# Performance work log

Hardware: AMD Instinct MI355X
Metric: run time of the kernel (lower is better)

The kernel has to match this reference:

```python
import jax, jax.numpy as jnp
import numpy as np

TOP_K = 2
CAPACITY_FACTOR = 1.25
AUX_LOSS_ALPHA = 0.01
Z_LOSS_ALPHA = 0.001


def setup_inputs() -> dict:
    key = jax.random.key(0)
    k1, k2, k3, k4 = jax.random.split(key, 4)
    B, S, H, I, E = 4, 2048, 1024, 4096, 8
    x = jax.random.normal(k1, (B, S, H), dtype=jnp.float32)
    # router: xavier_uniform with gain 0.1
    router_w = jax.random.normal(k2, (H, E), dtype=jnp.float32) * 0.1 * (2.0 / (H + E)) ** 0.5
    # expert weights: kaiming-ish scale 1/sqrt(fan_in)
    w1 = jax.random.normal(k3, (E, H, I), dtype=jnp.float32) * (1.0 / H) ** 0.5
    w2 = jax.random.normal(k4, (E, I, H), dtype=jnp.float32) * (1.0 / I) ** 0.5
    return {"x": x, "router_w": router_w, "w1": w1, "w2": w2}


def reference(x, router_w, w1, w2):
    B, S, H = x.shape
    E = router_w.shape[1]
    # router logits [B, S, E]
    logits = jnp.einsum('bsh,he->bse', x, router_w)
    # expert-choice: each expert picks `capacity` tokens along the seq axis
    capacity = int(min(S, max(1, (S * TOP_K) // E * CAPACITY_FACTOR)))
    topk_vals, topk_idx = jax.lax.top_k(jnp.swapaxes(logits, 1, 2), capacity)  # [B, E, C]
    topk_w = jax.nn.softmax(topk_vals, axis=-1)  # [B, E, C]
    # flat indices into [B*S] token space
    flat_idx = (jnp.arange(B)[:, None, None] * S + topk_idx).reshape(-1)  # [B*E*C]
    x_flat = x.reshape(-1, H)
    selected = x_flat[flat_idx].reshape(B, E, capacity, H)
    # per-expert SiLU MLP as grouped GEMMs
    mid = jax.nn.silu(jnp.einsum('bech,ehi->beci', selected, w1))
    expert_out = jnp.einsum('beci,eih->bech', mid, w2)
    weighted = (expert_out * topk_w[..., None]).reshape(-1, H)
    # scatter-add combine + count-based averaging
    out = jnp.zeros_like(x_flat).at[flat_idx].add(weighted)
    counts = jnp.zeros((B * S,), dtype=x.dtype).at[flat_idx].add(jnp.ones_like(flat_idx, dtype=x.dtype))
    out = (out / jnp.clip(counts, 1.0)[:, None]).reshape(B, S, H)
    # routing loss: load-balance aux + z-loss
    probs = jax.nn.softmax(logits, axis=-1)
    usage = probs.mean(axis=(0, 1))  # [E]
    aux_loss = jnp.mean((usage - 1.0 / E) ** 2) * E
    z_loss = jnp.mean(logits ** 2)
    routing_loss = AUX_LOSS_ALPHA * aux_loss + Z_LOSS_ALPHA * z_loss
    return out, routing_loss
```

## Files before the change

kernel.cpp:

```cpp
#include <hip/hip_runtime.h>
#include <hip/hip_bf16.h>
#include <stdint.h>

#define B_ 4
#define S_ 2048
#define H_ 1024
#define I_ 4096
#define E_ 8
#define CAP 640
#define NTOK (B_*S_)
#define NBE  (B_*E_)

typedef _Float16 f16;
typedef f16 f16x8 __attribute__((ext_vector_type(8)));
typedef float f32x4 __attribute__((ext_vector_type(4)));

#define OFF_LOGITS 0u
#define OFF_TOPKI  (256u*1024u)
#define OFF_TOPKW  (OFF_TOPKI + 128u*1024u)
#define OFF_COUNTS (OFF_TOPKW + 128u*1024u)
#define OFF_SCAL   (OFF_COUNTS + 64u*1024u)
#define OFF_XH     (1u<<20)
#define OFF_WT     (18u<<20)
#define OFF_MID    (86u<<20)

__device__ __forceinline__ void gl_lds16(const void* g, void* l) {
    __builtin_amdgcn_global_load_lds(
        (const __attribute__((address_space(1))) uint32_t*)g,
        (__attribute__((address_space(3))) uint32_t*)l, 16, 0, 0);
}

__global__ void k_router(const float* __restrict__ x, const float* __restrict__ rw,
                         float* __restrict__ logits, float* __restrict__ scal,
                         f16* __restrict__ xh) {
    __shared__ float rwt[E_ * H_];
    __shared__ float part[4][9];
    int tid = threadIdx.x;
    for (int i = tid; i < E_ * H_; i += 256) {
        int h = i >> 3, e = i & 7;
        rwt[e * H_ + h] = rw[i];
    }
    __syncthreads();
    int w = tid >> 6, lane = tid & 63;
    int t = blockIdx.x * 4 + w;
    const float* xr = x + (size_t)t * H_;
    f16* xhr = xh + ((size_t)t << 10);
    float acc[E_];
#pragma unroll
    for (int e = 0; e < E_; ++e) acc[e] = 0.f;
    for (int it = 0; it < H_ / 64; ++it) {
        int h = lane + it * 64;
        float xv = xr[h];
        xhr[h] = (f16)xv;
#pragma unroll
        for (int e = 0; e < E_; ++e) acc[e] += xv * rwt[e * H_ + h];
    }
#pragma unroll
    for (int off = 32; off > 0; off >>= 1)
#pragma unroll
        for (int e = 0; e < E_; ++e) acc[e] += __shfl_down(acc[e], off);
    if (lane == 0) {
        int b = t >> 11, s = t & 2047;
        float m = acc[0];
#pragma unroll
        for (int e = 1; e < E_; ++e) m = fmaxf(m, acc[e]);
        float z = 0.f, ps = 0.f;
        float p[E_];
#pragma unroll
        for (int e = 0; e < E_; ++e) {
            logits[(size_t)((b << 3) + e) * S_ + s] = acc[e];
            z += acc[e] * acc[e];
            p[e] = expf(acc[e] - m);
            ps += p[e];
        }
        part[w][0] = z;
#pragma unroll
        for (int e = 0; e < E_; ++e) part[w][1 + e] = p[e] / ps;
    }
    __syncthreads();
    if (tid < 9) {
        float v = part[0][tid] + part[1][tid] + part[2][tid] + part[3][tid];
        atomicAdd(&scal[tid], v);
    }
}

__global__ void __launch_bounds__(1024) k_topk(const float* __restrict__ logits,
                                               int* __restrict__ tki,
                                               float* __restrict__ tkw,
                                               float* __restrict__ counts) {
    int be = blockIdx.x;
    const float* row = logits + (size_t)be * S_;
    __shared__ unsigned hist[256];
    __shared__ unsigned long long wmax[16];
    __shared__ float wsum[16];
    __shared__ unsigned long long sh_prefix;
    __shared__ unsigned sh_rem;
    __shared__ unsigned long long sh_max;
    __shared__ float sh_stot;
    __shared__ unsigned sh_cnt;
    int tid = threadIdx.x;

    unsigned u0 = __float_as_uint(row[tid]);
    u0 = (u0 & 0x80000000u) ? ~u0 : (u0 | 0x80000000u);
    unsigned long long k0 = ((unsigned long long)u0 << 32) | (unsigned)(~tid);
    unsigned u1 = __float_as_uint(row[tid + 1024]);
    u1 = (u1 & 0x80000000u) ? ~u1 : (u1 | 0x80000000u);
    unsigned long long k1 = ((unsigned long long)u1 << 32) | (unsigned)(~(tid + 1024));

    if (tid == 0) { sh_cnt = 0; sh_rem = CAP; sh_prefix = 0; }
    unsigned long long m = k0 > k1 ? k0 : k1;
#pragma unroll
    for (int off = 32; off > 0; off >>= 1) {
        unsigned long long o = __shfl_down(m, off);
        if (o > m) m = o;
    }
    if ((tid & 63) == 0) wmax[tid >> 6] = m;
    __syncthreads();
    if (tid == 0) {
        unsigned long long mm = wmax[0];
#pragma unroll
        for (int i = 1; i < 16; ++i) if (wmax[i] > mm) mm = wmax[i];
        sh_max = mm;
    }

    unsigned long long prefix = 0;
    for (int L = 0; L < 8; ++L) {
        int shift = 56 - 8 * L;
        if (tid < 256) hist[tid] = 0;
        __syncthreads();
        bool m0 = (L == 0) || (((k0 ^ prefix) >> (shift + 8)) == 0);
        if (m0) atomicAdd(&hist[(unsigned)((k0 >> shift) & 255)], 1u);
        bool m1 = (L == 0) || (((k1 ^ prefix) >> (shift + 8)) == 0);
        if (m1) atomicAdd(&hist[(unsigned)((k1 >> shift) & 255)], 1u);
        __syncthreads();
        if (tid < 64) {
            unsigned g0 = hist[tid * 4], g1 = hist[tid * 4 + 1];
            unsigned g2 = hist[tid * 4 + 2], g3 = hist[tid * 4 + 3];
            unsigned gs = g0 + g1 + g2 + g3;
            unsigned suf = gs;
#pragma unroll
            for (int off = 1; off < 64; off <<= 1) {
                unsigned o = __shfl_down(suf, off);
                if (tid + off < 64) suf += o;
            }
            unsigned remaining = sh_rem;
            unsigned before = suf - gs;
            if (before < remaining && remaining <= suf) {
                unsigned cum = before;
                int bsel = tid * 4;
                unsigned rem2 = 0;
                for (int b = tid * 4 + 3; b >= tid * 4; --b) {
                    unsigned h = hist[b];
                    cum += h;
                    if (cum >= remaining) { bsel = b; rem2 = remaining - (cum - h); break; }
                }
                sh_prefix = prefix | ((unsigned long long)(unsigned)bsel << shift);
                sh_rem = rem2;
            }
        }
        __syncthreads();
        prefix = sh_prefix;
    }
    unsigned long long T = prefix;

    unsigned vu = (unsigned)(sh_max >> 32);
    float vmax = __uint_as_float((vu & 0x80000000u) ? (vu ^ 0x80000000u) : ~vu);

    float ex0 = 0.f, ex1 = 0.f;
    int idx0 = 0, idx1 = 0;
    if (k0 >= T) {
        idx0 = (int)(~(unsigned)k0) & 2047;
        unsigned vb = (unsigned)(k0 >> 32);
        float v = __uint_as_float((vb & 0x80000000u) ? (vb ^ 0x80000000u) : ~vb);
        ex0 = expf(v - vmax);
    }
    if (k1 >= T) {
        idx1 = (int)(~(unsigned)k1) & 2047;
        unsigned vb = (unsigned)(k1 >> 32);
        float v = __uint_as_float((vb & 0x80000000u) ? (vb ^ 0x80000000u) : ~vb);
        ex1 = expf(v - vmax);
    }
    float s = ex0 + ex1;
#pragma unroll
    for (int off = 32; off > 0; off >>= 1) s += __shfl_down(s, off);
    if ((tid & 63) == 0) wsum[tid >> 6] = s;
    __syncthreads();
    if (tid == 0) {
        float t2 = 0.f;
#pragma unroll
        for (int i = 0; i < 16; ++i) t2 += wsum[i];
        sh_stot = t2;
    }
    __syncthreads();
    float stot = sh_stot;
    if (k0 >= T) {
        unsigned slot = atomicAdd(&sh_cnt, 1u);
        tki[be * CAP + slot] = idx0;
        tkw[be * CAP + slot] = ex0 / stot;
        atomicAdd(&counts[(be >> 3) * S_ + idx0], 1.0f);
    }
    if (k1 >= T) {
        unsigned slot = atomicAdd(&sh_cnt, 1u);
        tki[be * CAP + slot] = idx1;
        tkw[be * CAP + slot] = ex1 / stot;
        atomicAdd(&counts[(be >> 3) * S_ + idx1], 1.0f);
    }
}

template<int R, int C>
__global__ void __launch_bounds__(256) k_transpose(const float* __restrict__ in,
                                                   f16* __restrict__ out) {
    __shared__ f16 t[64][68];
    int e = blockIdx.z;
    const float* ine = in + (size_t)e * R * C;
    f16* oute = out + (size_t)e * R * C;
    int c0 = blockIdx.x << 6, r0 = blockIdx.y << 6;
    int tx = threadIdx.x & 15, ty = threadIdx.x >> 4;
#pragma unroll
    for (int p = 0; p < 4; ++p) {
        int r = ty + p * 16;
        float4 v = *(const float4*)(ine + (size_t)(r0 + r) * C + c0 + tx * 4);
        t[tx * 4 + 0][r] = (f16)v.x;
        t[tx * 4 + 1][r] = (f16)v.y;
        t[tx * 4 + 2][r] = (f16)v.z;
        t[tx * 4 + 3][r] = (f16)v.w;
    }
    __syncthreads();
#pragma unroll
    for (int p = 0; p < 4; ++p) {
        int c = ty + p * 16;
        *(ushort4*)(oute + (size_t)(c0 + c) * R + r0 + tx * 4) =
            *(const ushort4*)&t[c][tx * 4];
    }
}


#define MFMA4(MI, A) \
    acc[MI][0] = __builtin_amdgcn_mfma_f32_16x16x32_f16(A, bf0, acc[MI][0], 0, 0, 0); \
    acc[MI][1] = __builtin_amdgcn_mfma_f32_16x16x32_f16(A, bf1, acc[MI][1], 0, 0, 0); \
    acc[MI][2] = __builtin_amdgcn_mfma_f32_16x16x32_f16(A, bf2, acc[MI][2], 0, 0, 0); \
    acc[MI][3] = __builtin_amdgcn_mfma_f32_16x16x32_f16(A, bf3, acc[MI][3], 0, 0, 0);

__global__ void __launch_bounds__(256, 4) k_gemm1(const f16* __restrict__ xh,
                                                  const f16* __restrict__ w1t,
                                                  const int* __restrict__ tki,
                                                  f16* __restrict__ mid) {
    __shared__ f16 As[128 * 64];
    __shared__ f16 Bs[128 * 64];
    int bid = blockIdx.x;
    int e = bid & 7;
    int r = bid >> 3;
    int rt = r % 20;
    int ct = r / 20;
    int n0 = ct << 7;
    const f16* w1e = w1t + ((size_t)e << 22);
    int tid = threadIdx.x;
    int w = tid >> 6, l = tid & 63;
    int wm = w >> 1, wn = w & 1;

    int gch = (tid & 7) ^ ((tid >> 3) & 7);
    int dstb = (tid >> 6) << 9;
    const f16* aS[4];
    const f16* bS[4];
#pragma unroll
    for (int i = 0; i < 4; ++i) {
        int ri = i * 32 + (tid >> 3);
        int ge = rt * 128 + ri;
        int bb = ge / 640;
        int cc = ge - bb * 640;
        int tok = tki[((bb << 3) + e) * 640 + cc];
        aS[i] = xh + ((size_t)((bb << 11) + tok) << 10) + (gch << 3);
        bS[i] = w1e + ((size_t)(n0 + ri) << 10) + (gch << 3);
    }

    int fr = l & 15, c4 = l >> 4;
    int f7 = fr & 7;
    int arow = (wm << 6) + fr;
    int brow = (wn << 6) + fr;
    f32x4 acc[4][4];
#pragma unroll
    for (int mi = 0; mi < 4; ++mi)
#pragma unroll
        for (int ni = 0; ni < 4; ++ni) acc[mi][ni] = (f32x4){0.f, 0.f, 0.f, 0.f};

    const int NT = H_ / 64;
    for (int t = 0; t < NT; ++t) {
        int ko = t << 6;
#pragma unroll
        for (int i = 0; i < 4; ++i) {
            gl_lds16(aS[i] + ko, As + i * 2048 + dstb);
            gl_lds16(bS[i] + ko, Bs + i * 2048 + dstb);
        }
        __syncthreads();
#pragma unroll
        for (int kf = 0; kf < 2; ++kf) {
            int sl = (((kf << 2) | c4) ^ f7) << 3;
            f16x8 bf0 = *(const f16x8*)(Bs + brow * 64 + sl);
            f16x8 bf1 = *(const f16x8*)(Bs + (brow + 16) * 64 + sl);
            f16x8 bf2 = *(const f16x8*)(Bs + (brow + 32) * 64 + sl);
            f16x8 bf3 = *(const f16x8*)(Bs + (brow + 48) * 64 + sl);
            f16x8 a0 = *(const f16x8*)(As + arow * 64 + sl);
            f16x8 a1 = *(const f16x8*)(As + (arow + 16) * 64 + sl);
            f16x8 a2 = *(const f16x8*)(As + (arow + 32) * 64 + sl);
            f16x8 a3 = *(const f16x8*)(As + (arow + 48) * 64 + sl);
            MFMA4(0, a0) MFMA4(1, a1) MFMA4(2, a2) MFMA4(3, a3)
        }
        __syncthreads();
    }

    int rq4 = c4 << 2;
#pragma unroll
    for (int mi = 0; mi < 4; ++mi) {
#pragma unroll
        for (int q = 0; q < 4; ++q) {
            int row = (wm << 6) + mi * 16 + rq4 + q;
            int ge = rt * 128 + row;
            int bb = ge / 640;
            int cc = ge - bb * 640;
            size_t flat = (size_t)(((bb << 3) + e) * 640 + cc);
            f16* mrow = mid + (flat << 12) + n0 + (wn << 6) + fr;
#pragma unroll
            for (int ni = 0; ni < 4; ++ni) {
                float v = acc[mi][ni][q];
                v = v / (1.f + expf(-v));
                mrow[ni * 16] = (f16)v;
            }
        }
    }
}

__global__ void __launch_bounds__(256, 4) k_gemm2(const f16* __restrict__ mid,
                                                  const f16* __restrict__ w2t,
                                                  const int* __restrict__ tki,
                                                  const float* __restrict__ tkw,
                                                  float* __restrict__ out) {
    __shared__ f16 As[128 * 64];
    __shared__ f16 Bs[128 * 64];
    int bid = blockIdx.x;
    int e = bid & 7;
    int r = bid >> 3;
    int rt = r % 20;
    int ct = r / 20;
    int n0 = ct << 7;
    const f16* w2e = w2t + ((size_t)e << 22);
    int tid = threadIdx.x;
    int w = tid >> 6, l = tid & 63;
    int wm = w >> 1, wn = w & 1;

    int gch = (tid & 7) ^ ((tid >> 3) & 7);
    int dstb = (tid >> 6) << 9;
    const f16* aS[4];
    const f16* bS[4];
#pragma unroll
    for (int i = 0; i < 4; ++i) {
        int ri = i * 32 + (tid >> 3);
        int ge = rt * 128 + ri;
        int bb = ge / 640;
        int cc = ge - bb * 640;
        size_t flat = (size_t)(((bb << 3) + e) * 640 + cc);
        aS[i] = mid + (flat << 12) + (gch << 3);
        bS[i] = w2e + ((size_t)(n0 + ri) << 12) + (gch << 3);
    }

    int fr = l & 15, c4 = l >> 4;
    int f7 = fr & 7;
    int arow = (wm << 6) + fr;
    int brow = (wn << 6) + fr;
    f32x4 acc[4][4];
#pragma unroll
    for (int mi = 0; mi < 4; ++mi)
#pragma unroll
        for (int ni = 0; ni < 4; ++ni) acc[mi][ni] = (f32x4){0.f, 0.f, 0.f, 0.f};

    const int NT = I_ / 64;
    for (int t = 0; t < NT; ++t) {
        int ko = t << 6;
#pragma unroll
        for (int i = 0; i < 4; ++i) {
            gl_lds16(aS[i] + ko, As + i * 2048 + dstb);
            gl_lds16(bS[i] + ko, Bs + i * 2048 + dstb);
        }
        __syncthreads();
#pragma unroll
        for (int kf = 0; kf < 2; ++kf) {
            int sl = (((kf << 2) | c4) ^ f7) << 3;
            f16x8 bf0 = *(const f16x8*)(Bs + brow * 64 + sl);
            f16x8 bf1 = *(const f16x8*)(Bs + (brow + 16) * 64 + sl);
            f16x8 bf2 = *(const f16x8*)(Bs + (brow + 32) * 64 + sl);
            f16x8 bf3 = *(const f16x8*)(Bs + (brow + 48) * 64 + sl);
            f16x8 a0 = *(const f16x8*)(As + arow * 64 + sl);
            f16x8 a1 = *(const f16x8*)(As + (arow + 16) * 64 + sl);
            f16x8 a2 = *(const f16x8*)(As + (arow + 32) * 64 + sl);
            f16x8 a3 = *(const f16x8*)(As + (arow + 48) * 64 + sl);
            MFMA4(0, a0) MFMA4(1, a1) MFMA4(2, a2) MFMA4(3, a3)
        }
        __syncthreads();
    }

    int* rowOffS = (int*)As;
    float* wtsS = (float*)(As + 256);
    if (tid < 128) {
        int ge = rt * 128 + tid;
        int bb = ge / 640;
        int cc = ge - bb * 640;
        int flat = ((bb << 3) + e) * 640 + cc;
        rowOffS[tid] = ((bb << 11) + tki[flat]) << 10;
        wtsS[tid] = tkw[flat];
    }
    __syncthreads();

    int rq4 = c4 << 2;
#pragma unroll
    for (int mi = 0; mi < 4; ++mi) {
#pragma unroll
        for (int q = 0; q < 4; ++q) {
            int row = (wm << 6) + mi * 16 + rq4 + q;
            int ro = rowOffS[row] + n0 + (wn << 6) + fr;
            float wg = wtsS[row];
#pragma unroll
            for (int ni = 0; ni < 4; ++ni) {
                atomicAdd(&out[ro + ni * 16], acc[mi][ni][q] * wg);
            }
        }
    }
}

__global__ void k_final(float* __restrict__ out, const float* __restrict__ counts,
                        const float* __restrict__ scal, float* __restrict__ loss_out) {
    size_t gid = (size_t)blockIdx.x * 256 + threadIdx.x;
    int tok = (int)(gid >> 8);
    float c = fmaxf(counts[tok], 1.0f);
    float4* o4 = (float4*)out;
    float4 v = o4[gid];
    v.x /= c; v.y /= c; v.z /= c; v.w /= c;
    o4[gid] = v;
    if (gid == 0) {
        float z = scal[0] / (float)(NTOK * E_);
        float aux = 0.f;
#pragma unroll
        for (int e = 0; e < E_; ++e) {
            float u = scal[1 + e] / (float)NTOK - 0.125f;
            aux += u * u;
        }
        loss_out[0] = 0.01f * aux + 0.001f * z;
    }
}

extern "C" void kernel_launch(void* const* d_in, const int* in_sizes, int n_in,
                              void* d_out, int out_size, void* d_ws, size_t ws_size,
                              hipStream_t stream) {
    const float* x  = (const float*)d_in[0];
    const float* rw = (const float*)d_in[1];
    const float* w1 = (const float*)d_in[2];
    const float* w2 = (const float*)d_in[3];
    float* out = (float*)d_out;
    char* ws = (char*)d_ws;

    float* logits = (float*)(ws + OFF_LOGITS);
    int*   tki    = (int*)(ws + OFF_TOPKI);
    float* tkw    = (float*)(ws + OFF_TOPKW);
    float* counts = (float*)(ws + OFF_COUNTS);
    float* scal   = (float*)(ws + OFF_SCAL);
    f16*   xh     = (f16*)(ws + OFF_XH);
    f16*   wt     = (f16*)(ws + OFF_WT);
    f16*   mid    = (f16*)(ws + OFF_MID);

    hipMemsetAsync(ws + OFF_COUNTS, 0, 64u * 1024u + 64u, stream);
    hipMemsetAsync(d_out, 0, (size_t)out_size * sizeof(float), stream);

    k_transpose<H_, I_><<<dim3(I_ / 64, H_ / 64, E_), 256, 0, stream>>>(w1, wt);
    k_router<<<NTOK / 4, 256, 0, stream>>>(x, rw, logits, scal, xh);
    k_topk<<<NBE, 1024, 0, stream>>>(logits, tki, tkw, counts);
    k_gemm1<<<5120, 256, 0, stream>>>(xh, wt, tki, mid);
    k_transpose<I_, H_><<<dim3(H_ / 64, I_ / 64, E_), 256, 0, stream>>>(w2, wt);
    k_gemm2<<<1280, 256, 0, stream>>>(mid, wt, tki, tkw, out);
    k_final<<<(NTOK * H_ / 4) / 256, 256, 0, stream>>>(out, counts, scal,
                                                       out + (size_t)NTOK * H_);
}
```

Baseline: 588.4 us.

## Rewrite gemm1 as 256x256 tile, 8-wave, double-buffered pipelined MFMA kernel

Replaces the 128x128 single-buffered gemm1 with a 256x256 output tile per 512-thread block. The new kernel uses double-buffered LDS, interleaves the global-to-LDS loads with MFMA phases, and places explicit barriers, vmcnt waits, sched barriers and setprio around each phase. The aim is to raise data reuse per loaded byte and hide global-load latency behind compute. In exchange it needs a large LDS footprint (128KB) and one block per CU, with hand-tuned waitcnt counts that must match the issue order exactly. gemm2 only gets its shared arrays renamed.

```diff
diff --git a/kernel.cpp b/kernel.cpp
--- a/kernel.cpp
+++ b/kernel.cpp
@@ -29,6 +29,10 @@
         (const __attribute__((address_space(1))) uint32_t*)g,
         (__attribute__((address_space(3))) uint32_t*)l, 16, 0, 0);
 }
+
+#define BAR()    asm volatile("s_barrier" ::: "memory")
+#define VMW(N)   asm volatile("s_waitcnt vmcnt(" #N ")" ::: "memory")
+#define SCHEDB() __builtin_amdgcn_sched_barrier(0)
 
 __global__ void k_router(const float* __restrict__ x, const float* __restrict__ rw,
                          float* __restrict__ logits, float* __restrict__ scal,
@@ -234,6 +238,162 @@
     }
 }
 
+#define MFMA_(A, B, C) __builtin_amdgcn_mfma_f32_16x16x32_f16(A, B, C, 0, 0, 0)
+
+__global__ void __launch_bounds__(512, 1) k_gemm1(const f16* __restrict__ xh,
+                                                  const f16* __restrict__ w1t,
+                                                  const int* __restrict__ tki,
+                                                  f16* __restrict__ mid) {
+    __shared__ f16 As[2 * 16384];
+    __shared__ f16 Bs[2 * 16384];
+    int bid = blockIdx.x;
+    int e = bid & 7;
+    int r = bid >> 3;
+    int mt = r % 10;
+    int ct = r / 10;
+    int n0 = ct << 8;
+    const f16* w1e = w1t + ((size_t)e << 22);
+    int tid = threadIdx.x;
+    int w = tid >> 6, l = tid & 63;
+    int wm = w >> 2, wn = w & 3;
+
+    int gch = (tid & 7) ^ ((tid >> 3) & 7);
+    const f16* aSrc[2][2];
+    const f16* bSrc[2][2];
+#pragma unroll
+    for (int h = 0; h < 2; ++h)
+#pragma unroll
+        for (int j = 0; j < 2; ++j) {
+            int rr = h * 128 + j * 64 + (tid >> 3);
+            int ge = mt * 256 + rr;
+            int bb = ge / 640, cc = ge - bb * 640;
+            int tok = tki[((bb << 3) + e) * 640 + cc];
+            aSrc[h][j] = xh + ((size_t)((bb << 11) + tok) << 10) + (gch << 3);
+            bSrc[h][j] = w1e + ((size_t)(n0 + rr) << 10) + (gch << 3);
+        }
+    int wdst = w << 9;
+
+#define SA(P, H, J, KO) gl_lds16(aSrc[H][J] + (KO), As + (P)*16384 + (H)*8192 + (J)*4096 + wdst)
+#define SB(P, H, J, KO) gl_lds16(bSrc[H][J] + (KO), Bs + (P)*16384 + (H)*8192 + (J)*4096 + wdst)
+
+    int fr = l & 15, c4 = l >> 4, f7 = fr & 7;
+    int sk0 = (c4 ^ f7) << 3;
+    int aOff = wm * 8192 + fr * 64 + sk0;
+    int bOff = (wn >> 1) * 8192 + (wn & 1) * 4096 + fr * 64 + sk0;
+    int aOff1 = aOff ^ 32, bOff1 = bOff ^ 32;
+
+    f32x4 acc[8][4];
+#pragma unroll
+    for (int mi = 0; mi < 8; ++mi)
+#pragma unroll
+        for (int ni = 0; ni < 4; ++ni) acc[mi][ni] = (f32x4){0.f, 0.f, 0.f, 0.f};
+
+    SB(0,0,0,0); SB(0,0,1,0); SB(0,1,0,0); SB(0,1,1,0);
+    SA(0,0,0,0); SA(0,0,1,0); SA(0,1,0,0); SA(0,1,1,0);
+    SB(1,0,0,64); SB(1,0,1,64); SB(1,1,0,64); SB(1,1,1,64);
+    VMW(4);
+    BAR();
+
+    f16x8 bfr[4][2];
+    f16x8 a0, a1, a2, a3;
+
+#define LDB(P) \
+    _Pragma("unroll") \
+    for (int ni = 0; ni < 4; ++ni) { \
+        bfr[ni][0] = *(const f16x8*)(Bs + (P)*16384 + bOff  + ni*1024); \
+        bfr[ni][1] = *(const f16x8*)(Bs + (P)*16384 + bOff1 + ni*1024); \
+    }
+#define LDA(P, M0) \
+    a0 = *(const f16x8*)(As + (P)*16384 + aOff  + (M0)*1024); \
+    a1 = *(const f16x8*)(As + (P)*16384 + aOff1 + (M0)*1024); \
+    a2 = *(const f16x8*)(As + (P)*16384 + aOff  + ((M0)+1)*1024); \
+    a3 = *(const f16x8*)(As + (P)*16384 + aOff1 + ((M0)+1)*1024);
+#define FMM(M0) \
+    __builtin_amdgcn_s_setprio(1); \
+    _Pragma("unroll") \
+    for (int ni = 0; ni < 4; ++ni) { \
+        acc[M0][ni]     = MFMA_(a0, bfr[ni][0], acc[M0][ni]); \
+        acc[M0][ni]     = MFMA_(a1, bfr[ni][1], acc[M0][ni]); \
+        acc[(M0)+1][ni] = MFMA_(a2, bfr[ni][0], acc[(M0)+1][ni]); \
+        acc[(M0)+1][ni] = MFMA_(a3, bfr[ni][1], acc[(M0)+1][ni]); \
+    } \
+    __builtin_amdgcn_s_setprio(0);
+
+#pragma unroll 1
+    for (int t = 0; t < 8; ++t) {
+        int koB = (2 * t + 1) << 6;
+        int k2 = 2 * t + 2; if (k2 > 15) k2 = 15;
+        int k3 = 2 * t + 3; if (k3 > 15) k3 = 15;
+        int ko2 = k2 << 6, ko3 = k3 << 6;
+        LDB(0); LDA(0, 0);
+        SA(1,0,0,koB); SA(1,0,1,koB);
+        BAR(); SCHEDB();
+        FMM(0);
+        BAR();
+        LDA(0, 2);
+        SA(1,1,0,koB); SA(1,1,1,koB);
+        SB(0,0,0,ko2); SB(0,0,1,ko2);
+        BAR(); SCHEDB();
+        FMM(2);
+        BAR();
+        LDA(0, 4);
+        SB(0,1,0,ko2); SB(0,1,1,ko2);
+        BAR(); SCHEDB();
+        FMM(4);
+        BAR();
+        LDA(0, 6);
+        BAR(); SCHEDB();
+        FMM(6);
+        VMW(4);
+        BAR();
+        LDB(1); LDA(1, 0);
+        SA(0,0,0,ko2); SA(0,0,1,ko2);
+        BAR(); SCHEDB();
+        FMM(0);
+        BAR();
+        LDA(1, 2);
+        SA(0,1,0,ko2); SA(0,1,1,ko2);
+        BAR(); SCHEDB();
+        FMM(2);
+        BAR();
+        LDA(1, 4);
+        SB(1,0,0,ko3); SB(1,0,1,ko3);
+        BAR(); SCHEDB();
+        FMM(4);
+        BAR();
+        LDA(1, 6);
+        SB(1,1,0,ko3); SB(1,1,1,ko3);
+        BAR(); SCHEDB();
+        FMM(6);
+        VMW(4);
+        BAR();
+    }
+#undef SA
+#undef SB
+#undef LDB
+#undef LDA
+#undef FMM
+
+    int rq4 = c4 << 2;
+#pragma unroll
+    for (int mi = 0; mi < 8; ++mi) {
+#pragma unroll
+        for (int q = 0; q < 4; ++q) {
+            int row = (wm << 7) + mi * 16 + rq4 + q;
+            int ge = mt * 256 + row;
+            int bb = ge / 640;
+            int cc = ge - bb * 640;
+            size_t flat = (size_t)(((bb << 3) + e) * 640 + cc);
+            f16* mrow = mid + (flat << 12) + n0 + (wn << 6) + fr;
+#pragma unroll
+            for (int ni = 0; ni < 4; ++ni) {
+                float v = acc[mi][ni][q];
+                v = v / (1.f + expf(-v));
+                mrow[ni * 16] = (f16)v;
+            }
+        }
+    }
+}
 
 #define MFMA4(MI, A) \
     acc[MI][0] = __builtin_amdgcn_mfma_f32_16x16x32_f16(A, bf0, acc[MI][0], 0, 0, 0); \
@@ -241,101 +401,13 @@
     acc[MI][2] = __builtin_amdgcn_mfma_f32_16x16x32_f16(A, bf2, acc[MI][2], 0, 0, 0); \
     acc[MI][3] = __builtin_amdgcn_mfma_f32_16x16x32_f16(A, bf3, acc[MI][3], 0, 0, 0);
 
-__global__ void __launch_bounds__(256, 4) k_gemm1(const f16* __restrict__ xh,
-                                                  const f16* __restrict__ w1t,
-                                                  const int* __restrict__ tki,
-                                                  f16* __restrict__ mid) {
-    __shared__ f16 As[128 * 64];
-    __shared__ f16 Bs[128 * 64];
-    int bid = blockIdx.x;
-    int e = bid & 7;
-    int r = bid >> 3;
-    int rt = r % 20;
-    int ct = r / 20;
-    int n0 = ct << 7;
-    const f16* w1e = w1t + ((size_t)e << 22);
-    int tid = threadIdx.x;
-    int w = tid >> 6, l = tid & 63;
-    int wm = w >> 1, wn = w & 1;
-
-    int gch = (tid & 7) ^ ((tid >> 3) & 7);
-    int dstb = (tid >> 6) << 9;
-    const f16* aS[4];
-    const f16* bS[4];
-#pragma unroll
-    for (int i = 0; i < 4; ++i) {
-        int ri = i * 32 + (tid >> 3);
-        int ge = rt * 128 + ri;
-        int bb = ge / 640;
-        int cc = ge - bb * 640;
-        int tok = tki[((bb << 3) + e) * 640 + cc];
-        aS[i] = xh + ((size_t)((bb << 11) + tok) << 10) + (gch << 3);
-        bS[i] = w1e + ((size_t)(n0 + ri) << 10) + (gch << 3);
-    }
-
-    int fr = l & 15, c4 = l >> 4;
-    int f7 = fr & 7;
-    int arow = (wm << 6) + fr;
-    int brow = (wn << 6) + fr;
-    f32x4 acc[4][4];
-#pragma unroll
-    for (int mi = 0; mi < 4; ++mi)
-#pragma unroll
-        for (int ni = 0; ni < 4; ++ni) acc[mi][ni] = (f32x4){0.f, 0.f, 0.f, 0.f};
-
-    const int NT = H_ / 64;
-    for (int t = 0; t < NT; ++t) {
-        int ko = t << 6;
-#pragma unroll
-        for (int i = 0; i < 4; ++i) {
-            gl_lds16(aS[i] + ko, As + i * 2048 + dstb);
-            gl_lds16(bS[i] + ko, Bs + i * 2048 + dstb);
-        }
-        __syncthreads();
-#pragma unroll
-        for (int kf = 0; kf < 2; ++kf) {
-            int sl = (((kf << 2) | c4) ^ f7) << 3;
-            f16x8 bf0 = *(const f16x8*)(Bs + brow * 64 + sl);
-            f16x8 bf1 = *(const f16x8*)(Bs + (brow + 16) * 64 + sl);
-            f16x8 bf2 = *(const f16x8*)(Bs + (brow + 32) * 64 + sl);
-            f16x8 bf3 = *(const f16x8*)(Bs + (brow + 48) * 64 + sl);
-            f16x8 a0 = *(const f16x8*)(As + arow * 64 + sl);
-            f16x8 a1 = *(const f16x8*)(As + (arow + 16) * 64 + sl);
-            f16x8 a2 = *(const f16x8*)(As + (arow + 32) * 64 + sl);
-            f16x8 a3 = *(const f16x8*)(As + (arow + 48) * 64 + sl);
-            MFMA4(0, a0) MFMA4(1, a1) MFMA4(2, a2) MFMA4(3, a3)
-        }
-        __syncthreads();
-    }
-
-    int rq4 = c4 << 2;
-#pragma unroll
-    for (int mi = 0; mi < 4; ++mi) {
-#pragma unroll
-        for (int q = 0; q < 4; ++q) {
-            int row = (wm << 6) + mi * 16 + rq4 + q;
-            int ge = rt * 128 + row;
-            int bb = ge / 640;
-            int cc = ge - bb * 640;
-            size_t flat = (size_t)(((bb << 3) + e) * 640 + cc);
-            f16* mrow = mid + (flat << 12) + n0 + (wn << 6) + fr;
-#pragma unroll
-            for (int ni = 0; ni < 4; ++ni) {
-                float v = acc[mi][ni][q];
-                v = v / (1.f + expf(-v));
-                mrow[ni * 16] = (f16)v;
-            }
-        }
-    }
-}
-
 __global__ void __launch_bounds__(256, 4) k_gemm2(const f16* __restrict__ mid,
                                                   const f16* __restrict__ w2t,
                                                   const int* __restrict__ tki,
                                                   const float* __restrict__ tkw,
                                                   float* __restrict__ out) {
-    __shared__ f16 As[128 * 64];
-    __shared__ f16 Bs[128 * 64];
+    __shared__ f16 As2[128 * 64];
+    __shared__ f16 Bs2[128 * 64];
     int bid = blockIdx.x;
     int e = bid & 7;
     int r = bid >> 3;
@@ -377,28 +449,28 @@
         int ko = t << 6;
 #pragma unroll
         for (int i = 0; i < 4; ++i) {
-            gl_lds16(aS[i] + ko, As + i * 2048 + dstb);
-            gl_lds16(bS[i] + ko, Bs + i * 2048 + dstb);
+            gl_lds16(aS[i] + ko, As2 + i * 2048 + dstb);
+            gl_lds16(bS[i] + ko, Bs2 + i * 2048 + dstb);
         }
         __syncthreads();
 #pragma unroll
         for (int kf = 0; kf < 2; ++kf) {
             int sl = (((kf << 2) | c4) ^ f7) << 3;
-            f16x8 bf0 = *(const f16x8*)(Bs + brow * 64 + sl);
-            f16x8 bf1 = *(const f16x8*)(Bs + (brow + 16) * 64 + sl);
-            f16x8 bf2 = *(const f16x8*)(Bs + (brow + 32) * 64 + sl);
-            f16x8 bf3 = *(const f16x8*)(Bs + (brow + 48) * 64 + sl);
-            f16x8 a0 = *(const f16x8*)(As + arow * 64 + sl);
-            f16x8 a1 = *(const f16x8*)(As + (arow + 16) * 64 + sl);
-            f16x8 a2 = *(const f16x8*)(As + (arow + 32) * 64 + sl);
-            f16x8 a3 = *(const f16x8*)(As + (arow + 48) * 64 + sl);
+            f16x8 bf0 = *(const f16x8*)(Bs2 + brow * 64 + sl);
+            f16x8 bf1 = *(const f16x8*)(Bs2 + (brow + 16) * 64 + sl);
+            f16x8 bf2 = *(const f16x8*)(Bs2 + (brow + 32) * 64 + sl);
+            f16x8 bf3 = *(const f16x8*)(Bs2 + (brow + 48) * 64 + sl);
+            f16x8 a0 = *(const f16x8*)(As2 + arow * 64 + sl);
+            f16x8 a1 = *(const f16x8*)(As2 + (arow + 16) * 64 + sl);
+            f16x8 a2 = *(const f16x8*)(As2 + (arow + 32) * 64 + sl);
+            f16x8 a3 = *(const f16x8*)(As2 + (arow + 48) * 64 + sl);
             MFMA4(0, a0) MFMA4(1, a1) MFMA4(2, a2) MFMA4(3, a3)
         }
         __syncthreads();
     }
 
-    int* rowOffS = (int*)As;
-    float* wtsS = (float*)(As + 256);
+    int* rowOffS = (int*)As2;
+    float* wtsS = (float*)(As2 + 256);
     if (tid < 128) {
         int ge = rt * 128 + tid;
         int bb = ge / 640;
@@ -471,7 +543,7 @@
     k_transpose<H_, I_><<<dim3(I_ / 64, H_ / 64, E_), 256, 0, stream>>>(w1, wt);
     k_router<<<NTOK / 4, 256, 0, stream>>>(x, rw, logits, scal, xh);
     k_topk<<<NBE, 1024, 0, stream>>>(logits, tki, tkw, counts);
-    k_gemm1<<<5120, 256, 0, stream>>>(xh, wt, tki, mid);
+    k_gemm1<<<1280, 512, 0, stream>>>(xh, wt, tki, mid);
     k_transpose<I_, H_><<<dim3(H_ / 64, I_ / 64, E_), 256, 0, stream>>>(w2, wt);
     k_gemm2<<<1280, 256, 0, stream>>>(mid, wt, tki, tkw, out);
     k_final<<<(NTOK * H_ / 4) / 256, 256, 0, stream>>>(out, counts, scal,
```

Result: slower. 607.2 us (+3.2%).

## Double-buffer LDS tiles with BK=32 in expert GEMMs to overlap loads and MFMA

Applied to the files above, without the earlier changes.

Both grouped GEMM kernels switch from a single 128x64 LDS tile with two barriers per k-step to double-buffered 128x32 tiles. The next tile's global-to-LDS loads are issued before the current tile's MFMAs, followed by one vmcnt wait and one barrier per step. The LDS swizzle is adjusted for the narrower rows. The SiLU epilogue also uses a fast exp and reciprocal. The trade-off is twice as many loop iterations with half the MFMA work each, so per-iteration barrier and wait overhead may dominate.

```diff
diff --git a/kernel.cpp b/kernel.cpp
--- a/kernel.cpp
+++ b/kernel.cpp
@@ -29,6 +29,9 @@
         (const __attribute__((address_space(1))) uint32_t*)g,
         (__attribute__((address_space(3))) uint32_t*)l, 16, 0, 0);
 }
+
+#define BAR()    asm volatile("s_barrier" ::: "memory")
+#define VMW0()   asm volatile("s_waitcnt vmcnt(0)" ::: "memory")
 
 __global__ void k_router(const float* __restrict__ x, const float* __restrict__ rw,
                          float* __restrict__ logits, float* __restrict__ scal,
@@ -245,8 +248,8 @@
                                                   const f16* __restrict__ w1t,
                                                   const int* __restrict__ tki,
                                                   f16* __restrict__ mid) {
-    __shared__ f16 As[128 * 64];
-    __shared__ f16 Bs[128 * 64];
+    __shared__ f16 As[2][4096];
+    __shared__ f16 Bs[2][4096];
     int bid = blockIdx.x;
     int e = bid & 7;
     int r = bid >> 3;
@@ -258,13 +261,13 @@
     int w = tid >> 6, l = tid & 63;
     int wm = w >> 1, wn = w & 1;
 
-    int gch = (tid & 7) ^ ((tid >> 3) & 7);
+    int gch = (tid & 3) ^ ((tid >> 2) & 3);
     int dstb = (tid >> 6) << 9;
-    const f16* aS[4];
-    const f16* bS[4];
-#pragma unroll
-    for (int i = 0; i < 4; ++i) {
-        int ri = i * 32 + (tid >> 3);
+    const f16* aS[2];
+    const f16* bS[2];
+#pragma unroll
+    for (int i = 0; i < 2; ++i) {
+        int ri = i * 64 + (tid >> 2);
         int ge = rt * 128 + ri;
         int bb = ge / 640;
         int cc = ge - bb * 640;
@@ -274,38 +277,38 @@
     }
 
     int fr = l & 15, c4 = l >> 4;
-    int f7 = fr & 7;
-    int arow = (wm << 6) + fr;
-    int brow = (wn << 6) + fr;
+    int sl = (c4 ^ (fr & 3)) << 3;
+    int arow = ((wm << 6) + fr) * 32 + sl;
+    int brow = ((wn << 6) + fr) * 32 + sl;
     f32x4 acc[4][4];
 #pragma unroll
     for (int mi = 0; mi < 4; ++mi)
 #pragma unroll
         for (int ni = 0; ni < 4; ++ni) acc[mi][ni] = (f32x4){0.f, 0.f, 0.f, 0.f};
 
-    const int NT = H_ / 64;
+    gl_lds16(aS[0], &As[0][dstb]);        gl_lds16(aS[1], &As[0][2048 + dstb]);
+    gl_lds16(bS[0], &Bs[0][dstb]);        gl_lds16(bS[1], &Bs[0][2048 + dstb]);
+    __syncthreads();
+
+    const int NT = H_ / 32;
     for (int t = 0; t < NT; ++t) {
-        int ko = t << 6;
-#pragma unroll
-        for (int i = 0; i < 4; ++i) {
-            gl_lds16(aS[i] + ko, As + i * 2048 + dstb);
-            gl_lds16(bS[i] + ko, Bs + i * 2048 + dstb);
-        }
-        __syncthreads();
-#pragma unroll
-        for (int kf = 0; kf < 2; ++kf) {
-            int sl = (((kf << 2) | c4) ^ f7) << 3;
-            f16x8 bf0 = *(const f16x8*)(Bs + brow * 64 + sl);
-            f16x8 bf1 = *(const f16x8*)(Bs + (brow + 16) * 64 + sl);
-            f16x8 bf2 = *(const f16x8*)(Bs + (brow + 32) * 64 + sl);
-            f16x8 bf3 = *(const f16x8*)(Bs + (brow + 48) * 64 + sl);
-            f16x8 a0 = *(const f16x8*)(As + arow * 64 + sl);
-            f16x8 a1 = *(const f16x8*)(As + (arow + 16) * 64 + sl);
-            f16x8 a2 = *(const f16x8*)(As + (arow + 32) * 64 + sl);
-            f16x8 a3 = *(const f16x8*)(As + (arow + 48) * 64 + sl);
-            MFMA4(0, a0) MFMA4(1, a1) MFMA4(2, a2) MFMA4(3, a3)
-        }
-        __syncthreads();
+        int cur = t & 1, nxt = cur ^ 1;
+        int ko = ((t < NT - 1) ? (t + 1) : t) << 5;
+        gl_lds16(aS[0] + ko, &As[nxt][dstb]);
+        gl_lds16(aS[1] + ko, &As[nxt][2048 + dstb]);
+        gl_lds16(bS[0] + ko, &Bs[nxt][dstb]);
+        gl_lds16(bS[1] + ko, &Bs[nxt][2048 + dstb]);
+        f16x8 bf0 = *(const f16x8*)(&Bs[cur][brow]);
+        f16x8 bf1 = *(const f16x8*)(&Bs[cur][brow + 512]);
+        f16x8 bf2 = *(const f16x8*)(&Bs[cur][brow + 1024]);
+        f16x8 bf3 = *(const f16x8*)(&Bs[cur][brow + 1536]);
+        f16x8 a0 = *(const f16x8*)(&As[cur][arow]);
+        f16x8 a1 = *(const f16x8*)(&As[cur][arow + 512]);
+        f16x8 a2 = *(const f16x8*)(&As[cur][arow + 1024]);
+        f16x8 a3 = *(const f16x8*)(&As[cur][arow + 1536]);
+        MFMA4(0, a0) MFMA4(1, a1) MFMA4(2, a2) MFMA4(3, a3)
+        VMW0();
+        BAR();
     }
 
     int rq4 = c4 << 2;
@@ -322,7 +325,7 @@
 #pragma unroll
             for (int ni = 0; ni < 4; ++ni) {
                 float v = acc[mi][ni][q];
-                v = v / (1.f + expf(-v));
+                v = v * __builtin_amdgcn_rcpf(1.f + __expf(-v));
                 mrow[ni * 16] = (f16)v;
             }
         }
@@ -334,8 +337,8 @@
                                                   const int* __restrict__ tki,
                                                   const float* __restrict__ tkw,
                                                   float* __restrict__ out) {
-    __shared__ f16 As[128 * 64];
-    __shared__ f16 Bs[128 * 64];
+    __shared__ f16 As2[2][4096];
+    __shared__ f16 Bs2[2][4096];
     int bid = blockIdx.x;
     int e = bid & 7;
     int r = bid >> 3;
@@ -347,13 +350,13 @@
     int w = tid >> 6, l = tid & 63;
     int wm = w >> 1, wn = w & 1;
 
-    int gch = (tid & 7) ^ ((tid >> 3) & 7);
+    int gch = (tid & 3) ^ ((tid >> 2) & 3);
     int dstb = (tid >> 6) << 9;
-    const f16* aS[4];
-    const f16* bS[4];
-#pragma unroll
-    for (int i = 0; i < 4; ++i) {
-        int ri = i * 32 + (tid >> 3);
+    const f16* aS[2];
+    const f16* bS[2];
+#pragma unroll
+    for (int i = 0; i < 2; ++i) {
+        int ri = i * 64 + (tid >> 2);
         int ge = rt * 128 + ri;
         int bb = ge / 640;
         int cc = ge - bb * 640;
@@ -363,42 +366,42 @@
     }
 
     int fr = l & 15, c4 = l >> 4;
-    int f7 = fr & 7;
-    int arow = (wm << 6) + fr;
-    int brow = (wn << 6) + fr;
+    int sl = (c4 ^ (fr & 3)) << 3;
+    int arow = ((wm << 6) + fr) * 32 + sl;
+    int brow = ((wn << 6) + fr) * 32 + sl;
     f32x4 acc[4][4];
 #pragma unroll
     for (int mi = 0; mi < 4; ++mi)
 #pragma unroll
         for (int ni = 0; ni < 4; ++ni) acc[mi][ni] = (f32x4){0.f, 0.f, 0.f, 0.f};
 
-    const int NT = I_ / 64;
+    gl_lds16(aS[0], &As2[0][dstb]);       gl_lds16(aS[1], &As2[0][2048 + dstb]);
+    gl_lds16(bS[0], &Bs2[0][dstb]);       gl_lds16(bS[1], &Bs2[0][2048 + dstb]);
+    __syncthreads();
+
+    const int NT = I_ / 32;
     for (int t = 0; t < NT; ++t) {
-        int ko = t << 6;
-#pragma unroll
-        for (int i = 0; i < 4; ++i) {
-            gl_lds16(aS[i] + ko, As + i * 2048 + dstb);
-            gl_lds16(bS[i] + ko, Bs + i * 2048 + dstb);
-        }
-        __syncthreads();
-#pragma unroll
-        for (int kf = 0; kf < 2; ++kf) {
-            int sl = (((kf << 2) | c4) ^ f7) << 3;
-            f16x8 bf0 = *(const f16x8*)(Bs + brow * 64 + sl);
-            f16x8 bf1 = *(const f16x8*)(Bs + (brow + 16) * 64 + sl);
-            f16x8 bf2 = *(const f16x8*)(Bs + (brow + 32) * 64 + sl);
-            f16x8 bf3 = *(const f16x8*)(Bs + (brow + 48) * 64 + sl);
-            f16x8 a0 = *(const f16x8*)(As + arow * 64 + sl);
-            f16x8 a1 = *(const f16x8*)(As + (arow + 16) * 64 + sl);
-            f16x8 a2 = *(const f16x8*)(As + (arow + 32) * 64 + sl);
-            f16x8 a3 = *(const f16x8*)(As + (arow + 48) * 64 + sl);
-            MFMA4(0, a0) MFMA4(1, a1) MFMA4(2, a2) MFMA4(3, a3)
-        }
-        __syncthreads();
-    }
-
-    int* rowOffS = (int*)As;
-    float* wtsS = (float*)(As + 256);
+        int cur = t & 1, nxt = cur ^ 1;
+        int ko = ((t < NT - 1) ? (t + 1) : t) << 5;
+        gl_lds16(aS[0] + ko, &As2[nxt][dstb]);
+        gl_lds16(aS[1] + ko, &As2[nxt][2048 + dstb]);
+        gl_lds16(bS[0] + ko, &Bs2[nxt][dstb]);
+        gl_lds16(bS[1] + ko, &Bs2[nxt][2048 + dstb]);
+        f16x8 bf0 = *(const f16x8*)(&Bs2[cur][brow]);
+        f16x8 bf1 = *(const f16x8*)(&Bs2[cur][brow + 512]);
+        f16x8 bf2 = *(const f16x8*)(&Bs2[cur][brow + 1024]);
+        f16x8 bf3 = *(const f16x8*)(&Bs2[cur][brow + 1536]);
+        f16x8 a0 = *(const f16x8*)(&As2[cur][arow]);
+        f16x8 a1 = *(const f16x8*)(&As2[cur][arow + 512]);
+        f16x8 a2 = *(const f16x8*)(&As2[cur][arow + 1024]);
+        f16x8 a3 = *(const f16x8*)(&As2[cur][arow + 1536]);
+        MFMA4(0, a0) MFMA4(1, a1) MFMA4(2, a2) MFMA4(3, a3)
+        VMW0();
+        BAR();
+    }
+
+    int* rowOffS = (int*)&As2[0][0];
+    float* wtsS = (float*)&As2[0][256];
     if (tid < 128) {
         int ge = rt * 128 + tid;
         int bb = ge / 640;
```

Result: slower. 654.0 us (+11.2%).
